# Kernel optimization log

Measured on AMD Instinct MI355X. Metric: run time of the kernel, lower is better.

Reference implementation:

```python
import jax, jax.numpy as jnp
import numpy as np
from jax import lax

PAD_IDX = 0
SOS_IDX = 1


def gru_cell(x, h, w_ih, w_hh, b_ih, b_hh):
    # PyTorch GRU cell: gates ordered [r, z, n]
    gi = x @ w_ih.T + b_ih            # [B, 3H]
    gh = h @ w_hh.T + b_hh            # [B, 3H]
    i_r, i_z, i_n = jnp.split(gi, 3, axis=-1)
    h_r, h_z, h_n = jnp.split(gh, 3, axis=-1)
    r = jax.nn.sigmoid(i_r + h_r)
    z = jax.nn.sigmoid(i_z + h_z)
    n = jnp.tanh(i_n + r * h_n)
    return (1.0 - z) * n + z * h


def setup_inputs() -> dict:
    key = jax.random.key(0)
    ks = jax.random.split(key, 24)
    B, S, T = 32, 64, 48
    Vs, Vt, E, H = 32000, 32000, 512, 1024
    sH = 1.0 / np.sqrt(H)
    sE = 1.0 / np.sqrt(E)

    def p(k, shape, scale):
        return jax.random.normal(k, shape, jnp.float32) * scale

    inp = {
        'source_ids': jax.random.randint(ks[0], (B, S), 0, Vs),
        'target_ids': jax.random.randint(ks[1], (B, T), 0, Vt),
        'enc_embed': p(ks[2], (Vs, E), 0.02).at[PAD_IDX].set(0.0),
        'enc_w_ih': p(ks[3], (3 * H, E), sE),
        'enc_w_hh': p(ks[4], (3 * H, H), sH),
        'enc_b_ih': p(ks[5], (3 * H,), sH),
        'enc_b_hh': p(ks[6], (3 * H,), sH),
        'wq': p(ks[7], (H, H), sH),
        'bq': p(ks[8], (H,), sH),
        'wk': p(ks[9], (H, H), sH),
        'bk': p(ks[10], (H,), sH),
        'ws': p(ks[11], (H,), sH),
        'bs': p(ks[12], (), sH),
        'dec_embed': p(ks[13], (Vt, E), 0.02).at[PAD_IDX].set(0.0),
        'dec_w_ih': p(ks[14], (3 * H, E + H), sH),
        'dec_w_hh': p(ks[15], (3 * H, H), sH),
        'dec_b_ih': p(ks[16], (3 * H,), sH),
        'dec_b_hh': p(ks[17], (3 * H,), sH),
        'wo': p(ks[18], (Vt, H), sH),
        'bo': p(ks[19], (Vt,), sH),
    }
    return inp


def reference(source_ids, target_ids, enc_embed, enc_w_ih, enc_w_hh, enc_b_ih,
              enc_b_hh, wq, bq, wk, bk, ws, bs, dec_embed, dec_w_ih, dec_w_hh,
              dec_b_ih, dec_b_hh, wo, bo):
    B, S = source_ids.shape
    T = target_ids.shape[1]
    H = wq.shape[0]

    # ----- encoder GRU -----
    enc_emb = enc_embed[source_ids]                  # [B,S,E] (dropout = identity, eval)
    h0 = jnp.zeros((B, H), enc_emb.dtype)

    def enc_step(h, x):
        h = gru_cell(x, h, enc_w_ih, enc_w_hh, enc_b_ih, enc_b_hh)
        return h, h

    h_final, enc_out = lax.scan(enc_step, h0, enc_emb.transpose(1, 0, 2))
    enc_out = enc_out.transpose(1, 0, 2)             # [B,S,H]

    mask = source_ids != PAD_IDX                     # [B,S]
    keys_proj = enc_out @ wk.T + bk                  # [B,S,H] (hoisted; linear, step-invariant)

    # ----- decoder with teacher forcing (ratio=1.0 => always teacher) -----
    dec_in = jnp.concatenate(
        [jnp.full((B, 1), SOS_IDX, dtype=target_ids.dtype), target_ids[:, 1:T - 1]],
        axis=1)                                      # [B,T-1]
    dec_emb = dec_embed[dec_in].transpose(1, 0, 2)   # [T-1,B,E]

    def dec_step(h, emb):
        q = h @ wq.T + bq                            # [B,H]
        scores = jnp.tanh(q[:, None, :] + keys_proj) @ ws + bs   # [B,S]
        scores = jnp.where(mask, scores, -jnp.inf)
        w = jax.nn.softmax(scores, axis=-1)          # [B,S]
        ctx = jnp.einsum('bs,bsh->bh', w, enc_out)   # [B,H]
        x = jnp.concatenate([emb, ctx], axis=-1)     # [B,E+H]
        h2 = gru_cell(x, h, dec_w_ih, dec_w_hh, dec_b_ih, dec_b_hh)
        logits = h2 @ wo.T + bo                      # [B,V]
        return h2, (logits, w)

    _, (logits, attn) = lax.scan(dec_step, h_final, dec_emb)
    logits = logits.transpose(1, 0, 2)               # [B,T-1,V]
    attn = attn.transpose(1, 0, 2)                   # [B,T-1,S]
    return logits, attn
```

## Files before the change

kernel.cpp:

```cpp
#include <hip/hip_runtime.h>


#define BB 32
#define SS 64
#define TT 48
#define TD 47
#define EE 512
#define HH 1024
#define GG 3072
#define VV 32000
#define SOS_IDX 1
#define MPAD 1536

typedef float f32x4 __attribute__((ext_vector_type(4)));
typedef short bf16x8 __attribute__((ext_vector_type(8)));

static __device__ __forceinline__ float sigmoid_f(float x) {
    return 1.0f / (1.0f + __expf(-x));
}
static __device__ __forceinline__ float tanh_f(float x) {
    return 1.0f - 2.0f / (__expf(2.0f * x) + 1.0f);
}
static __device__ __forceinline__ unsigned short f2bf(float f) {
    unsigned u = __float_as_uint(f);
    u = u + 0x7fffu + ((u >> 16) & 1u);
    return (unsigned short)(u >> 16);
}
static __device__ __forceinline__ void cst4(float* p, f32x4 v) {
    asm volatile("global_store_dwordx4 %0, %1, off sc0 sc1" :: "v"(p), "v"(v) : "memory");
}
static __device__ __forceinline__ void cst1(float* p, float v) {
    asm volatile("global_store_dword %0, %1, off sc0 sc1" :: "v"(p), "v"(v) : "memory");
}

static __device__ __forceinline__ void gbar(int* bar, int leafsz, int& bstep) {
    asm volatile("s_waitcnt vmcnt(0) lgkmcnt(0)" ::: "memory");
    __syncthreads();
    bstep += 1;
    if (threadIdx.x == 0) {
        int* leaf = bar + (blockIdx.x & 7) * 32;
        int* root = bar + 512;
        int lv = __hip_atomic_fetch_add(leaf, 1, __ATOMIC_RELAXED, __HIP_MEMORY_SCOPE_AGENT) + 1;
        if (lv == bstep * leafsz) {
            __hip_atomic_fetch_add(root, 1, __ATOMIC_RELAXED, __HIP_MEMORY_SCOPE_AGENT);
        }
        while (__hip_atomic_load(root, __ATOMIC_RELAXED, __HIP_MEMORY_SCOPE_AGENT) < bstep * 8) {
            __builtin_amdgcn_s_sleep(1);
        }
    }
    __syncthreads();
    asm volatile("" ::: "memory");
}

__global__ void k_dec_idx(const int* __restrict__ tgt, int* __restrict__ idx) {
    int m = blockIdx.x * 256 + threadIdx.x;
    if (m < TD * BB) {
        int t = m >> 5, b = m & 31;
        idx[m] = (t == 0) ? SOS_IDX : tgt[b * TT + t];
    }
}

__global__ __launch_bounds__(256) void k_gemm128(
    const float* __restrict__ A, const float* __restrict__ Wt,
    const float* __restrict__ bias, float* __restrict__ C,
    const int* __restrict__ rowidx,
    int M, int N, int K, int lda, int ldw, int ldc)
{
    __shared__ __align__(16) float As[16][128];
    __shared__ __align__(16) float Bs[16][128];
    const int tid = threadIdx.x;
    const int tm = tid >> 4, tn = tid & 15;
    const int row0 = blockIdx.y * 128;
    const int col0 = blockIdx.x * 128;
    const int lr = tid >> 1;
    const int lq = tid & 1;

    long arow_off = -1;
    {
        int arow = row0 + lr;
        if (arow < M) {
            int r = rowidx ? rowidx[arow] : arow;
            arow_off = (long)r * lda;
        }
    }
    const long wrow_off = (long)(col0 + lr) * ldw;

    float acc[8][8];
#pragma unroll
    for (int i = 0; i < 8; ++i)
#pragma unroll
        for (int j = 0; j < 8; ++j) acc[i][j] = 0.f;

    for (int k0 = 0; k0 < K; k0 += 16) {
        f32x4 av0 = {0.f,0.f,0.f,0.f}, av1 = {0.f,0.f,0.f,0.f};
        if (arow_off >= 0) {
            av0 = *(const f32x4*)(A + arow_off + k0 + lq * 8);
            av1 = *(const f32x4*)(A + arow_off + k0 + lq * 8 + 4);
        }
        f32x4 wv0 = *(const f32x4*)(Wt + wrow_off + k0 + lq * 8);
        f32x4 wv1 = *(const f32x4*)(Wt + wrow_off + k0 + lq * 8 + 4);
        __syncthreads();
#pragma unroll
        for (int i = 0; i < 4; ++i) {
            As[lq * 8 + i][lr] = av0[i];
            As[lq * 8 + 4 + i][lr] = av1[i];
            Bs[lq * 8 + i][lr] = wv0[i];
            Bs[lq * 8 + 4 + i][lr] = wv1[i];
        }
        __syncthreads();
#pragma unroll
        for (int kk = 0; kk < 16; ++kk) {
            f32x4 a0 = *(const f32x4*)&As[kk][tm * 4];
            f32x4 a1 = *(const f32x4*)&As[kk][64 + tm * 4];
            f32x4 b0 = *(const f32x4*)&Bs[kk][tn * 4];
            f32x4 b1 = *(const f32x4*)&Bs[kk][64 + tn * 4];
            float a[8], b[8];
#pragma unroll
            for (int i = 0; i < 4; ++i) {
                a[i] = a0[i]; a[4 + i] = a1[i];
                b[i] = b0[i]; b[4 + i] = b1[i];
            }
#pragma unroll
            for (int i = 0; i < 8; ++i)
#pragma unroll
                for (int j = 0; j < 8; ++j) acc[i][j] += a[i] * b[j];
        }
    }

    f32x4 bv0 = {0.f,0.f,0.f,0.f}, bv1 = {0.f,0.f,0.f,0.f};
    if (bias) {
        bv0 = *(const f32x4*)(bias + col0 + tn * 4);
        bv1 = *(const f32x4*)(bias + col0 + 64 + tn * 4);
    }
#pragma unroll
    for (int i = 0; i < 8; ++i) {
        int m = row0 + ((i < 4) ? (tm * 4 + i) : (64 + tm * 4 + i - 4));
        if (m >= M) continue;
        f32x4 v0, v1;
#pragma unroll
        for (int j = 0; j < 4; ++j) {
            v0[j] = acc[i][j] + bv0[j];
            v1[j] = acc[i][4 + j] + bv1[j];
        }
        *(f32x4*)(C + (long)m * ldc + col0 + tn * 4) = v0;
        *(f32x4*)(C + (long)m * ldc + col0 + 64 + tn * 4) = v1;
    }
}

__global__ __launch_bounds__(256) void k_cvtA(
    const float* __restrict__ A, unsigned short* __restrict__ Ah,
    unsigned short* __restrict__ Al)
{
    size_t i4 = ((size_t)blockIdx.x * 256 + threadIdx.x) * 4;
    int row = (int)(i4 >> 10);
    f32x4 v = {0.f, 0.f, 0.f, 0.f};
    if (row < TD * BB) v = *(const f32x4*)(A + i4);
    ushort4 h, l;
    float hf;
    h.x = f2bf(v.x); hf = __uint_as_float((unsigned)h.x << 16); l.x = f2bf(v.x - hf);
    h.y = f2bf(v.y); hf = __uint_as_float((unsigned)h.y << 16); l.y = f2bf(v.y - hf);
    h.z = f2bf(v.z); hf = __uint_as_float((unsigned)h.z << 16); l.z = f2bf(v.z - hf);
    h.w = f2bf(v.w); hf = __uint_as_float((unsigned)h.w << 16); l.w = f2bf(v.w - hf);
    *(ushort4*)(Ah + i4) = h;
    *(ushort4*)(Al + i4) = l;
}

__global__ __launch_bounds__(256) void k_cvtB(
    const float* __restrict__ Bsrc, unsigned short* __restrict__ Bh)
{
    size_t i4 = ((size_t)blockIdx.x * 256 + threadIdx.x) * 4;
    f32x4 v = *(const f32x4*)(Bsrc + i4);
    ushort4 h;
    h.x = f2bf(v.x); h.y = f2bf(v.y); h.z = f2bf(v.z); h.w = f2bf(v.w);
    *(ushort4*)(Bh + i4) = h;
}

__global__ __launch_bounds__(256) void k_mfma_logits(
    const unsigned short* __restrict__ Ah,
    const unsigned short* __restrict__ Bh,
    const float* __restrict__ bo, float* __restrict__ C)
{
    __shared__ __align__(16) unsigned short As[128 * 64];
    __shared__ __align__(16) unsigned short Bs[128 * 64];
    const int tid = threadIdx.x;
    const int m0 = blockIdx.y * 128;
    const int n0 = blockIdx.x * 128;
    const int r = tid >> 1, half = tid & 1;
    const int lane = tid & 63, wid = tid >> 6;
    const int wm = wid >> 1, wn = wid & 1;

    f32x4 acc[4][4];
#pragma unroll
    for (int i = 0; i < 4; ++i)
#pragma unroll
        for (int j = 0; j < 4; ++j) acc[i][j] = (f32x4){0.f, 0.f, 0.f, 0.f};

    char* AsB = (char*)As;
    char* BsB = (char*)Bs;
    const int lwb = r * 128 + half * 64;
    const int swz = (r & 7) << 4;

    for (int kt = 0; kt < 32; ++kt) {
        const int kb = (kt & 15) * 64;
        const unsigned short* Ap = Ah + ((kt >> 4) ? (size_t)MPAD * 1024 : 0)
                                 + (size_t)(m0 + r) * 1024 + kb + half * 32;
        const unsigned short* Bp = Bh + (size_t)(n0 + r) * 1024 + kb + half * 32;
        f32x4 a0 = *(const f32x4*)(Ap + 0);
        f32x4 a1 = *(const f32x4*)(Ap + 8);
        f32x4 a2 = *(const f32x4*)(Ap + 16);
        f32x4 a3 = *(const f32x4*)(Ap + 24);
        f32x4 b0 = *(const f32x4*)(Bp + 0);
        f32x4 b1 = *(const f32x4*)(Bp + 8);
        f32x4 b2 = *(const f32x4*)(Bp + 16);
        f32x4 b3 = *(const f32x4*)(Bp + 24);
        __syncthreads();
        *(f32x4*)(AsB + ((lwb + 0)  ^ swz)) = a0;
        *(f32x4*)(AsB + ((lwb + 16) ^ swz)) = a1;
        *(f32x4*)(AsB + ((lwb + 32) ^ swz)) = a2;
        *(f32x4*)(AsB + ((lwb + 48) ^ swz)) = a3;
        *(f32x4*)(BsB + ((lwb + 0)  ^ swz)) = b0;
        *(f32x4*)(BsB + ((lwb + 16) ^ swz)) = b1;
        *(f32x4*)(BsB + ((lwb + 32) ^ swz)) = b2;
        *(f32x4*)(BsB + ((lwb + 48) ^ swz)) = b3;
        __syncthreads();
#pragma unroll
        for (int ks = 0; ks < 2; ++ks) {
            bf16x8 af[4], bf[4];
#pragma unroll
            for (int u = 0; u < 4; ++u) {
                int ml = wm * 64 + u * 16 + (lane & 15);
                int byteA = ml * 128 + ks * 64 + ((lane >> 4) << 4);
                af[u] = *(const bf16x8*)(AsB + (byteA ^ ((ml & 7) << 4)));
                int nl = wn * 64 + u * 16 + (lane & 15);
                int byteB = nl * 128 + ks * 64 + ((lane >> 4) << 4);
                bf[u] = *(const bf16x8*)(BsB + (byteB ^ ((nl & 7) << 4)));
            }
#pragma unroll
            for (int mi = 0; mi < 4; ++mi)
#pragma unroll
                for (int ni = 0; ni < 4; ++ni)
                    acc[mi][ni] = __builtin_amdgcn_mfma_f32_16x16x32_bf16(
                        af[mi], bf[ni], acc[mi][ni], 0, 0, 0);
        }
    }

    const int cl = lane & 15, rq = lane >> 4;
#pragma unroll
    for (int ni = 0; ni < 4; ++ni) {
        int col = n0 + wn * 64 + ni * 16 + cl;
        float bias = bo[col];
#pragma unroll
        for (int mi = 0; mi < 4; ++mi) {
#pragma unroll
            for (int j = 0; j < 4; ++j) {
                int m = m0 + wm * 64 + mi * 16 + rq * 4 + j;
                if (m < TD * BB) {
                    int orow = (m & 31) * TD + (m >> 5);
                    C[(size_t)orow * VV + col] = acc[mi][ni][j] + bias;
                }
            }
        }
    }
}

__global__ __launch_bounds__(512, 2) void k_enc_steps(
    const float* __restrict__ gi, const float* __restrict__ Whh,
    const float* __restrict__ bhh, float* __restrict__ enc_out,
    int s0, int ns, int* bar)
{
    __shared__ float red[12][16][32];
    __shared__ float sums[12][32];
    const int tid = threadIdx.x, bid = blockIdx.x;
    const int b = tid & 31, ks = tid >> 5;
    const int j0 = bid * 4;
    const int kc = ks * 64;
    int bstep = 0;

    for (int ss = 0; ss < ns; ++ss) {
        const int s = s0 + ss;
        float acc[12];
#pragma unroll
        for (int u = 0; u < 12; ++u) acc[u] = 0.f;
        if (s > 0) {
            f32x4 hreg[16];
            const float* hb = enc_out + ((size_t)b * SS + (s - 1)) * HH + kc;
#pragma unroll
            for (int i = 0; i < 16; ++i) hreg[i] = *(const f32x4*)(hb + (i << 2));
#pragma unroll
            for (int jj = 0; jj < 4; ++jj) {
                const float* pr = Whh + ((size_t)(j0 + jj) << 10) + kc;
                const float* pz = Whh + ((size_t)(HH + j0 + jj) << 10) + kc;
                const float* pn = Whh + ((size_t)(2 * HH + j0 + jj) << 10) + kc;
                float ar = 0.f, az = 0.f, an = 0.f;
#pragma unroll
                for (int i = 0; i < 16; ++i) {
                    f32x4 h4 = hreg[i];
                    f32x4 w;
                    w = *(const f32x4*)(pr + (i << 2));
                    ar += h4.x * w.x + h4.y * w.y + h4.z * w.z + h4.w * w.w;
                    w = *(const f32x4*)(pz + (i << 2));
                    az += h4.x * w.x + h4.y * w.y + h4.z * w.z + h4.w * w.w;
                    w = *(const f32x4*)(pn + (i << 2));
                    an += h4.x * w.x + h4.y * w.y + h4.z * w.z + h4.w * w.w;
                }
                acc[jj] = ar; acc[4 + jj] = az; acc[8 + jj] = an;
            }
        }
#pragma unroll
        for (int u = 0; u < 12; ++u) red[u][ks][b] = acc[u];
        __syncthreads();
        if (tid < 384) {
            int u = tid >> 5, fb = tid & 31;
            float x = 0.f;
#pragma unroll
            for (int q = 0; q < 16; ++q) x += red[u][q][fb];
            sums[u][fb] = x;
        }
        __syncthreads();
        if (tid < 32) {
            const f32x4 bh0 = *(const f32x4*)(bhh + j0);
            const f32x4 bh1 = *(const f32x4*)(bhh + HH + j0);
            const f32x4 bh2 = *(const f32x4*)(bhh + 2 * HH + j0);
            const float* gr = gi + (size_t)(tid * SS + s) * GG;
            f32x4 g0 = *(const f32x4*)(gr + j0);
            f32x4 g1 = *(const f32x4*)(gr + HH + j0);
            f32x4 g2 = *(const f32x4*)(gr + 2 * HH + j0);
            f32x4 hold = {0.f, 0.f, 0.f, 0.f};
            if (s > 0) hold = *(const f32x4*)(enc_out + ((size_t)tid * SS + (s - 1)) * HH + j0);
            f32x4 hn;
#pragma unroll
            for (int e = 0; e < 4; ++e) {
                float r = sigmoid_f(g0[e] + sums[e][tid] + bh0[e]);
                float z = sigmoid_f(g1[e] + sums[4 + e][tid] + bh1[e]);
                float n = tanh_f(g2[e] + r * (sums[8 + e][tid] + bh2[e]));
                hn[e] = (1.f - z) * n + z * hold[e];
            }
            cst4(enc_out + ((size_t)tid * SS + s) * HH + j0, hn);
        }
        if (ss != ns - 1) gbar(bar, 256 / 8, bstep);
    }
}

__global__ __launch_bounds__(512, 2) void k_dec_step(
    const float* __restrict__ hbase, long hstride,
    const float* __restrict__ Whh, const float* __restrict__ wq,
    const float* __restrict__ bq, const float* __restrict__ keys,
    const float* __restrict__ wsv, const float* __restrict__ bsv,
    const int* __restrict__ src, const float* __restrict__ encproj,
    const float* __restrict__ gi, const float* __restrict__ bhh,
    float* __restrict__ q2, float* __restrict__ hsums2,
    float* __restrict__ h2all, float* __restrict__ attn_out,
    int t, int* bar)
{
    __shared__ float red[16][16][32];
    __shared__ float qsum[4][32];
    const int tid = threadIdx.x, bid = blockIdx.x;
    const int b = tid & 31, ks = tid >> 5;
    const int j0 = bid * 4;
    const int kc = ks * 64;
    int bstep = 0;

    {
        f32x4 hreg[16];
        const float* hb = hbase + (size_t)b * hstride + kc;
#pragma unroll
        for (int i = 0; i < 16; ++i) hreg[i] = *(const f32x4*)(hb + (i << 2));
        float acc[16];
#pragma unroll
        for (int jj = 0; jj < 4; ++jj) {
            const float* pr = Whh + ((size_t)(j0 + jj) << 10) + kc;
            const float* pz = Whh + ((size_t)(HH + j0 + jj) << 10) + kc;
            const float* pn = Whh + ((size_t)(2 * HH + j0 + jj) << 10) + kc;
            const float* pq = wq + ((size_t)(j0 + jj) << 10) + kc;
            float ar = 0.f, az = 0.f, an = 0.f, aq = 0.f;
#pragma unroll
            for (int i = 0; i < 16; ++i) {
                f32x4 h4 = hreg[i];
                f32x4 w;
                w = *(const f32x4*)(pr + (i << 2));
                ar += h4.x * w.x + h4.y * w.y + h4.z * w.z + h4.w * w.w;
                w = *(const f32x4*)(pz + (i << 2));
                az += h4.x * w.x + h4.y * w.y + h4.z * w.z + h4.w * w.w;
                w = *(const f32x4*)(pn + (i << 2));
                an += h4.x * w.x + h4.y * w.y + h4.z * w.z + h4.w * w.w;
                w = *(const f32x4*)(pq + (i << 2));
                aq += h4.x * w.x + h4.y * w.y + h4.z * w.z + h4.w * w.w;
            }
            acc[jj] = ar; acc[4 + jj] = az; acc[8 + jj] = an; acc[12 + jj] = aq;
        }
#pragma unroll
        for (int u = 0; u < 16; ++u) red[u][ks][b] = acc[u];
        __syncthreads();
        {
            int u = tid >> 5, fb = tid & 31;
            float x = 0.f;
#pragma unroll
            for (int q = 0; q < 16; ++q) x += red[u][q][fb];
            if (u < 12) cst1(hsums2 + (size_t)bid * 384 + u * 32 + fb, x);
            else qsum[u - 12][fb] = x;
        }
        __syncthreads();
        if (tid < 32) {
            const f32x4 bq4 = *(const f32x4*)(bq + j0);
            f32x4 qv;
            qv.x = qsum[0][tid] + bq4.x;
            qv.y = qsum[1][tid] + bq4.y;
            qv.z = qsum[2][tid] + bq4.z;
            qv.w = qsum[3][tid] + bq4.w;
            cst4(q2 + (size_t)bid * 128 + tid * 4, qv);
        }
    }
    gbar(bar, 256 / 8, bstep);

    const int ab = bid & 31, part = bid >> 5;
    float* qs  = &red[0][0][0];
    float* wss = qs + 1024;
    float* scs = wss + 1024;
    float* wl  = scs + 512;
    float* xls = wl + 64;
    if (tid < 256) {
        f32x4 qv = *(const f32x4*)(q2 + (size_t)tid * 128 + ab * 4);
        f32x4 wv = *(const f32x4*)(wsv + tid * 4);
        *(f32x4*)&qs[tid * 4] = qv;
        *(f32x4*)&wss[tid * 4] = wv;
    }
    __syncthreads();
    {
        const int s4 = tid >> 3, kq = tid & 7;
        const float* kr = keys + (size_t)(ab * SS + s4) * HH + kq * 128;
        float a = 0.f;
        for (int i = 0; i < 32; ++i) {
            f32x4 kv = *(const f32x4*)(kr + (i << 2));
            int k = kq * 128 + (i << 2);
            a += tanh_f(qs[k] + kv.x) * wss[k]
               + tanh_f(qs[k + 1] + kv.y) * wss[k + 1]
               + tanh_f(qs[k + 2] + kv.z) * wss[k + 2]
               + tanh_f(qs[k + 3] + kv.w) * wss[k + 3];
        }
        scs[kq * 64 + s4] = a;
    }
    __syncthreads();
    if (tid < 64) {
        float v = bsv[0];
#pragma unroll
        for (int q = 0; q < 8; ++q) v += scs[q * 64 + tid];
        bool valid = src[ab * SS + tid] != 0;
        float m = valid ? v : -3.0e38f;
        for (int off = 32; off; off >>= 1) m = fmaxf(m, __shfl_xor(m, off));
        float e = valid ? __expf(v - m) : 0.f;
        float ssum = e;
        for (int off = 32; off; off >>= 1) ssum += __shfl_xor(ssum, off);
        float wgt = e / ssum;
        wl[tid] = wgt;
        if (part == 0)
            attn_out[((size_t)ab * TD + t) * SS + tid] = wgt;
    }
    __syncthreads();
    if (tid < 384) {
        int gate = tid >> 7, jj = tid & 127;
        int col = (gate << 10) + (part << 7) + jj;
        float xa = 0.f;
        const float* ep = encproj + (size_t)ab * SS * GG + col;
        for (int s2 = 0; s2 < 64; ++s2)
            xa += wl[s2] * ep[(size_t)s2 * GG];
        xls[tid] = xa;
    }
    __syncthreads();
    if (tid < 128) {
        const int j = (part << 7) + tid;
        const int wbid = (part << 5) + (tid >> 2);
        const int jj = tid & 3;
        const float* hs = hsums2 + (size_t)wbid * 384;
        float sh0 = hs[(0 * 4 + jj) * 32 + ab];
        float sh1 = hs[(1 * 4 + jj) * 32 + ab];
        float sh2 = hs[(2 * 4 + jj) * 32 + ab];
        const float* gr = gi + (size_t)(t * BB + ab) * GG;
        float r = sigmoid_f(gr[j] + xls[tid] + sh0 + bhh[j]);
        float z = sigmoid_f(gr[HH + j] + xls[128 + tid] + sh1 + bhh[HH + j]);
        float n = tanh_f(gr[2 * HH + j] + xls[256 + tid] + r * (sh2 + bhh[2 * HH + j]));
        float hold = hbase[(size_t)ab * hstride + j];
        h2all[((size_t)t * BB + ab) * HH + j] = (1.f - z) * n + z * hold;
    }
}

extern "C" void kernel_launch(void* const* d_in, const int* in_sizes, int n_in,
                              void* d_out, int out_size, void* d_ws, size_t ws_size,
                              hipStream_t stream)
{
    const int*   src  = (const int*)d_in[0];
    const int*   tgt  = (const int*)d_in[1];
    const float* eemb = (const float*)d_in[2];
    const float* ewih = (const float*)d_in[3];
    const float* ewhh = (const float*)d_in[4];
    const float* ebih = (const float*)d_in[5];
    const float* ebhh = (const float*)d_in[6];
    const float* wq   = (const float*)d_in[7];
    const float* bq   = (const float*)d_in[8];
    const float* wk   = (const float*)d_in[9];
    const float* bk   = (const float*)d_in[10];
    const float* wsv  = (const float*)d_in[11];
    const float* bsv  = (const float*)d_in[12];
    const float* demb = (const float*)d_in[13];
    const float* dwih = (const float*)d_in[14];
    const float* dwhh = (const float*)d_in[15];
    const float* dbih = (const float*)d_in[16];
    const float* dbhh = (const float*)d_in[17];
    const float* wo   = (const float*)d_in[18];
    const float* bo   = (const float*)d_in[19];
    float* out = (float*)d_out;

    float* w = (float*)d_ws;
    float* enc_gi  = w;
    float* dec_gi  = enc_gi  + (size_t)BB * SS * GG;
    float* enc_out = dec_gi  + (size_t)TD * BB * GG;
    float* keys    = enc_out + (size_t)BB * SS * HH;
    float* h2all   = keys    + (size_t)BB * SS * HH;
    float* q2      = h2all   + (size_t)TD * BB * HH;
    float* hsums2  = q2      + (size_t)256 * 128;
    int*   didx    = (int*)(hsums2 + (size_t)256 * 384);
    int*   barAll  = didx + TD * BB + 32;
    unsigned short* Ah = (unsigned short*)(barAll + 63 * 576 + 32);
    unsigned short* Al = Ah + (size_t)MPAD * 1024;
    unsigned short* Bh = (unsigned short*)w;

    float* encproj = enc_gi;
    float* attn_out = out + (size_t)BB * TD * VV;

    hipMemsetAsync(barAll, 0, 63 * 576 * sizeof(int), stream);
    k_dec_idx<<<dim3((TD * BB + 255) / 256), 256, 0, stream>>>(tgt, didx);

    k_gemm128<<<dim3(GG / 128, (BB * SS) / 128), 256, 0, stream>>>(
        eemb, ewih, ebih, enc_gi, src, BB * SS, GG, EE, EE, EE, GG);
    k_gemm128<<<dim3(GG / 128, (TD * BB + 127) / 128), 256, 0, stream>>>(
        demb, dwih, dbih, dec_gi, didx, TD * BB, GG, EE, EE, EE + HH, GG);

    for (int i = 0; i < 16; ++i)
        k_enc_steps<<<dim3(256), dim3(512), 0, stream>>>(
            enc_gi, ewhh, ebhh, enc_out, i * 4, 4, barAll + i * 576);

    k_gemm128<<<dim3(HH / 128, (BB * SS) / 128), 256, 0, stream>>>(
        enc_out, wk, bk, keys, nullptr, BB * SS, HH, HH, HH, HH, HH);
    k_gemm128<<<dim3(GG / 128, (BB * SS) / 128), 256, 0, stream>>>(
        enc_out, dwih + EE, nullptr, encproj, nullptr,
        BB * SS, GG, HH, HH, EE + HH, GG);

    for (int t = 0; t < TD; ++t) {
        const float* hbase = (t == 0) ? enc_out + (size_t)(SS - 1) * HH
                                      : h2all + (size_t)(t - 1) * BB * HH;
        long hstride = (t == 0) ? (long)SS * HH : (long)HH;
        k_dec_step<<<dim3(256), dim3(512), 0, stream>>>(
            hbase, hstride, dwhh, wq, bq, keys, wsv, bsv, src, encproj,
            dec_gi, dbhh, q2, hsums2, h2all, attn_out, t, barAll + (16 + t) * 576);
    }

    k_cvtA<<<dim3(MPAD * 1024 / 1024), 256, 0, stream>>>(h2all, Ah, Al);
    k_cvtB<<<dim3(VV * 1024 / 1024), 256, 0, stream>>>(wo, Bh);
    k_mfma_logits<<<dim3(VV / 128, MPAD / 128), 256, 0, stream>>>(
        Ah, Bh, bo, out);
}
```

Before: 4.588 ms.

## Make encoder and decoder recurrences persistent kernels with grid barriers

Replaces the 16 encoder launches and 47 per-step decoder launches with one persistent kernel each, which loops over all timesteps and synchronises through the existing atomic grid barrier. Cross-block values (q2, hsums2, h2all) are now read and written with cache-bypassing loads and stores so they stay visible between steps without a kernel boundary. The ws vector is loaded into shared memory once per kernel rather than once per step. This removes per-launch overhead and the launch gaps between steps, but it depends on all 256 blocks being resident at once and adds one extra barrier per decoder step.

```diff
diff --git a/kernel.cpp b/kernel.cpp
--- a/kernel.cpp
+++ b/kernel.cpp
@@ -31,6 +31,20 @@
 }
 static __device__ __forceinline__ void cst1(float* p, float v) {
     asm volatile("global_store_dword %0, %1, off sc0 sc1" :: "v"(p), "v"(v) : "memory");
+}
+static __device__ __forceinline__ f32x4 cld4(const float* p) {
+    f32x4 v;
+    asm volatile("global_load_dwordx4 %0, %1, off sc0 sc1" : "=v"(v) : "v"(p) : "memory");
+    return v;
+}
+static __device__ __forceinline__ float cld1f(const float* p) {
+    float v;
+    asm volatile("global_load_dword %0, %1, off sc0 sc1" : "=v"(v) : "v"(p) : "memory");
+    return v;
+}
+static __device__ __forceinline__ void cwait() {
+    asm volatile("s_waitcnt vmcnt(0)" ::: "memory");
+    __builtin_amdgcn_sched_barrier(0);
 }
 
 static __device__ __forceinline__ void gbar(int* bar, int leafsz, int& bstep) {
@@ -263,10 +277,9 @@
     }
 }
 
-__global__ __launch_bounds__(512, 2) void k_enc_steps(
+__global__ __launch_bounds__(512, 2) void k_enc_all(
     const float* __restrict__ gi, const float* __restrict__ Whh,
-    const float* __restrict__ bhh, float* __restrict__ enc_out,
-    int s0, int ns, int* bar)
+    const float* __restrict__ bhh, float* __restrict__ enc_out, int* bar)
 {
     __shared__ float red[12][16][32];
     __shared__ float sums[12][32];
@@ -276,8 +289,7 @@
     const int kc = ks * 64;
     int bstep = 0;
 
-    for (int ss = 0; ss < ns; ++ss) {
-        const int s = s0 + ss;
+    for (int s = 0; s < SS; ++s) {
         float acc[12];
 #pragma unroll
         for (int u = 0; u < 12; ++u) acc[u] = 0.f;
@@ -337,149 +349,160 @@
             }
             cst4(enc_out + ((size_t)tid * SS + s) * HH + j0, hn);
         }
-        if (ss != ns - 1) gbar(bar, 256 / 8, bstep);
-    }
-}
-
-__global__ __launch_bounds__(512, 2) void k_dec_step(
-    const float* __restrict__ hbase, long hstride,
-    const float* __restrict__ Whh, const float* __restrict__ wq,
-    const float* __restrict__ bq, const float* __restrict__ keys,
-    const float* __restrict__ wsv, const float* __restrict__ bsv,
-    const int* __restrict__ src, const float* __restrict__ encproj,
-    const float* __restrict__ gi, const float* __restrict__ bhh,
-    float* __restrict__ q2, float* __restrict__ hsums2,
-    float* __restrict__ h2all, float* __restrict__ attn_out,
-    int t, int* bar)
+        if (s != SS - 1) gbar(bar, 256 / 8, bstep);
+    }
+}
+
+__global__ __launch_bounds__(512, 2) void k_dec_all(
+    const float* __restrict__ enc_out, const float* __restrict__ Whh,
+    const float* __restrict__ wq, const float* __restrict__ bq,
+    const float* __restrict__ keys, const float* __restrict__ wsv,
+    const float* __restrict__ bsv, const int* __restrict__ src,
+    const float* __restrict__ encproj, const float* __restrict__ gi,
+    const float* __restrict__ bhh, float* __restrict__ q2,
+    float* __restrict__ hsums2, float* __restrict__ h2all,
+    float* __restrict__ attn_out, int* bar)
 {
     __shared__ float red[16][16][32];
     __shared__ float qsum[4][32];
+    __shared__ float wss[HH];
     const int tid = threadIdx.x, bid = blockIdx.x;
     const int b = tid & 31, ks = tid >> 5;
     const int j0 = bid * 4;
     const int kc = ks * 64;
+    const int ab = bid & 31, part = bid >> 5;
     int bstep = 0;
 
-    {
-        f32x4 hreg[16];
-        const float* hb = hbase + (size_t)b * hstride + kc;
-#pragma unroll
-        for (int i = 0; i < 16; ++i) hreg[i] = *(const f32x4*)(hb + (i << 2));
-        float acc[16];
-#pragma unroll
-        for (int jj = 0; jj < 4; ++jj) {
-            const float* pr = Whh + ((size_t)(j0 + jj) << 10) + kc;
-            const float* pz = Whh + ((size_t)(HH + j0 + jj) << 10) + kc;
-            const float* pn = Whh + ((size_t)(2 * HH + j0 + jj) << 10) + kc;
-            const float* pq = wq + ((size_t)(j0 + jj) << 10) + kc;
-            float ar = 0.f, az = 0.f, an = 0.f, aq = 0.f;
-#pragma unroll
-            for (int i = 0; i < 16; ++i) {
-                f32x4 h4 = hreg[i];
-                f32x4 w;
-                w = *(const f32x4*)(pr + (i << 2));
-                ar += h4.x * w.x + h4.y * w.y + h4.z * w.z + h4.w * w.w;
-                w = *(const f32x4*)(pz + (i << 2));
-                az += h4.x * w.x + h4.y * w.y + h4.z * w.z + h4.w * w.w;
-                w = *(const f32x4*)(pn + (i << 2));
-                an += h4.x * w.x + h4.y * w.y + h4.z * w.z + h4.w * w.w;
-                w = *(const f32x4*)(pq + (i << 2));
-                aq += h4.x * w.x + h4.y * w.y + h4.z * w.z + h4.w * w.w;
-            }
-            acc[jj] = ar; acc[4 + jj] = az; acc[8 + jj] = an; acc[12 + jj] = aq;
-        }
-#pragma unroll
-        for (int u = 0; u < 16; ++u) red[u][ks][b] = acc[u];
-        __syncthreads();
+    if (tid < 256)
+        *(f32x4*)&wss[tid * 4] = *(const f32x4*)(wsv + tid * 4);
+    const f32x4 bq4 = *(const f32x4*)(bq + j0);
+
+    for (int t = 0; t < TD; ++t) {
+        const float* hbase = (t == 0) ? enc_out + (size_t)(SS - 1) * HH
+                                      : h2all + (size_t)(t - 1) * BB * HH;
+        const long hstride = (t == 0) ? (long)SS * HH : (long)HH;
+
         {
-            int u = tid >> 5, fb = tid & 31;
-            float x = 0.f;
-#pragma unroll
-            for (int q = 0; q < 16; ++q) x += red[u][q][fb];
-            if (u < 12) cst1(hsums2 + (size_t)bid * 384 + u * 32 + fb, x);
-            else qsum[u - 12][fb] = x;
-        }
-        __syncthreads();
-        if (tid < 32) {
-            const f32x4 bq4 = *(const f32x4*)(bq + j0);
-            f32x4 qv;
-            qv.x = qsum[0][tid] + bq4.x;
-            qv.y = qsum[1][tid] + bq4.y;
-            qv.z = qsum[2][tid] + bq4.z;
-            qv.w = qsum[3][tid] + bq4.w;
-            cst4(q2 + (size_t)bid * 128 + tid * 4, qv);
-        }
-    }
-    gbar(bar, 256 / 8, bstep);
-
-    const int ab = bid & 31, part = bid >> 5;
-    float* qs  = &red[0][0][0];
-    float* wss = qs + 1024;
-    float* scs = wss + 1024;
-    float* wl  = scs + 512;
-    float* xls = wl + 64;
-    if (tid < 256) {
-        f32x4 qv = *(const f32x4*)(q2 + (size_t)tid * 128 + ab * 4);
-        f32x4 wv = *(const f32x4*)(wsv + tid * 4);
-        *(f32x4*)&qs[tid * 4] = qv;
-        *(f32x4*)&wss[tid * 4] = wv;
-    }
-    __syncthreads();
-    {
-        const int s4 = tid >> 3, kq = tid & 7;
-        const float* kr = keys + (size_t)(ab * SS + s4) * HH + kq * 128;
-        float a = 0.f;
-        for (int i = 0; i < 32; ++i) {
-            f32x4 kv = *(const f32x4*)(kr + (i << 2));
-            int k = kq * 128 + (i << 2);
-            a += tanh_f(qs[k] + kv.x) * wss[k]
-               + tanh_f(qs[k + 1] + kv.y) * wss[k + 1]
-               + tanh_f(qs[k + 2] + kv.z) * wss[k + 2]
-               + tanh_f(qs[k + 3] + kv.w) * wss[k + 3];
-        }
-        scs[kq * 64 + s4] = a;
-    }
-    __syncthreads();
-    if (tid < 64) {
-        float v = bsv[0];
-#pragma unroll
-        for (int q = 0; q < 8; ++q) v += scs[q * 64 + tid];
-        bool valid = src[ab * SS + tid] != 0;
-        float m = valid ? v : -3.0e38f;
-        for (int off = 32; off; off >>= 1) m = fmaxf(m, __shfl_xor(m, off));
-        float e = valid ? __expf(v - m) : 0.f;
-        float ssum = e;
-        for (int off = 32; off; off >>= 1) ssum += __shfl_xor(ssum, off);
-        float wgt = e / ssum;
-        wl[tid] = wgt;
-        if (part == 0)
-            attn_out[((size_t)ab * TD + t) * SS + tid] = wgt;
-    }
-    __syncthreads();
-    if (tid < 384) {
-        int gate = tid >> 7, jj = tid & 127;
-        int col = (gate << 10) + (part << 7) + jj;
-        float xa = 0.f;
-        const float* ep = encproj + (size_t)ab * SS * GG + col;
-        for (int s2 = 0; s2 < 64; ++s2)
-            xa += wl[s2] * ep[(size_t)s2 * GG];
-        xls[tid] = xa;
-    }
-    __syncthreads();
-    if (tid < 128) {
-        const int j = (part << 7) + tid;
-        const int wbid = (part << 5) + (tid >> 2);
-        const int jj = tid & 3;
-        const float* hs = hsums2 + (size_t)wbid * 384;
-        float sh0 = hs[(0 * 4 + jj) * 32 + ab];
-        float sh1 = hs[(1 * 4 + jj) * 32 + ab];
-        float sh2 = hs[(2 * 4 + jj) * 32 + ab];
-        const float* gr = gi + (size_t)(t * BB + ab) * GG;
-        float r = sigmoid_f(gr[j] + xls[tid] + sh0 + bhh[j]);
-        float z = sigmoid_f(gr[HH + j] + xls[128 + tid] + sh1 + bhh[HH + j]);
-        float n = tanh_f(gr[2 * HH + j] + xls[256 + tid] + r * (sh2 + bhh[2 * HH + j]));
-        float hold = hbase[(size_t)ab * hstride + j];
-        h2all[((size_t)t * BB + ab) * HH + j] = (1.f - z) * n + z * hold;
+            f32x4 hreg[16];
+            const float* hb = hbase + (size_t)b * hstride + kc;
+#pragma unroll
+            for (int i = 0; i < 16; ++i) hreg[i] = *(const f32x4*)(hb + (i << 2));
+            float acc[16];
+#pragma unroll
+            for (int jj = 0; jj < 4; ++jj) {
+                const float* pr = Whh + ((size_t)(j0 + jj) << 10) + kc;
+                const float* pz = Whh + ((size_t)(HH + j0 + jj) << 10) + kc;
+                const float* pn = Whh + ((size_t)(2 * HH + j0 + jj) << 10) + kc;
+                const float* pq = wq + ((size_t)(j0 + jj) << 10) + kc;
+                float ar = 0.f, az = 0.f, an = 0.f, aq = 0.f;
+#pragma unroll
+                for (int i = 0; i < 16; ++i) {
+                    f32x4 h4 = hreg[i];
+                    f32x4 w;
+                    w = *(const f32x4*)(pr + (i << 2));
+                    ar += h4.x * w.x + h4.y * w.y + h4.z * w.z + h4.w * w.w;
+                    w = *(const f32x4*)(pz + (i << 2));
+                    az += h4.x * w.x + h4.y * w.y + h4.z * w.z + h4.w * w.w;
+                    w = *(const f32x4*)(pn + (i << 2));
+                    an += h4.x * w.x + h4.y * w.y + h4.z * w.z + h4.w * w.w;
+                    w = *(const f32x4*)(pq + (i << 2));
+                    aq += h4.x * w.x + h4.y * w.y + h4.z * w.z + h4.w * w.w;
+                }
+                acc[jj] = ar; acc[4 + jj] = az; acc[8 + jj] = an; acc[12 + jj] = aq;
+            }
+#pragma unroll
+            for (int u = 0; u < 16; ++u) red[u][ks][b] = acc[u];
+            __syncthreads();
+            {
+                int u = tid >> 5, fb = tid & 31;
+                float x = 0.f;
+#pragma unroll
+                for (int q = 0; q < 16; ++q) x += red[u][q][fb];
+                if (u < 12) cst1(hsums2 + (size_t)bid * 384 + u * 32 + fb, x);
+                else qsum[u - 12][fb] = x;
+            }
+            __syncthreads();
+            if (tid < 32) {
+                f32x4 qv;
+                qv.x = qsum[0][tid] + bq4.x;
+                qv.y = qsum[1][tid] + bq4.y;
+                qv.z = qsum[2][tid] + bq4.z;
+                qv.w = qsum[3][tid] + bq4.w;
+                cst4(q2 + (size_t)bid * 128 + tid * 4, qv);
+            }
+        }
+        gbar(bar, 256 / 8, bstep);
+
+        {
+            float* qs  = &red[0][0][0];
+            float* scs = qs + 1024;
+            float* wl  = scs + 512;
+            float* xls = wl + 64;
+            if (tid < 256) {
+                f32x4 qv = cld4(q2 + (size_t)tid * 128 + ab * 4);
+                cwait();
+                *(f32x4*)&qs[tid * 4] = qv;
+            }
+            __syncthreads();
+            {
+                const int s4 = tid >> 3, kq = tid & 7;
+                const float* kr = keys + (size_t)(ab * SS + s4) * HH + kq * 128;
+                float a = 0.f;
+                for (int i = 0; i < 32; ++i) {
+                    f32x4 kv = *(const f32x4*)(kr + (i << 2));
+                    int k = kq * 128 + (i << 2);
+                    a += tanh_f(qs[k] + kv.x) * wss[k]
+                       + tanh_f(qs[k + 1] + kv.y) * wss[k + 1]
+                       + tanh_f(qs[k + 2] + kv.z) * wss[k + 2]
+                       + tanh_f(qs[k + 3] + kv.w) * wss[k + 3];
+                }
+                scs[kq * 64 + s4] = a;
+            }
+            __syncthreads();
+            if (tid < 64) {
+                float v = bsv[0];
+#pragma unroll
+                for (int q = 0; q < 8; ++q) v += scs[q * 64 + tid];
+                bool valid = src[ab * SS + tid] != 0;
+                float m = valid ? v : -3.0e38f;
+                for (int off = 32; off; off >>= 1) m = fmaxf(m, __shfl_xor(m, off));
+                float e = valid ? __expf(v - m) : 0.f;
+                float ssum = e;
+                for (int off = 32; off; off >>= 1) ssum += __shfl_xor(ssum, off);
+                float wgt = e / ssum;
+                wl[tid] = wgt;
+                if (part == 0)
+                    attn_out[((size_t)ab * TD + t) * SS + tid] = wgt;
+            }
+            __syncthreads();
+            if (tid < 384) {
+                int gate = tid >> 7, jj = tid & 127;
+                int col = (gate << 10) + (part << 7) + jj;
+                float xa = 0.f;
+                const float* ep = encproj + (size_t)ab * SS * GG + col;
+                for (int s2 = 0; s2 < 64; ++s2)
+                    xa += wl[s2] * ep[(size_t)s2 * GG];
+                xls[tid] = xa;
+            }
+            __syncthreads();
+            if (tid < 128) {
+                const int j = (part << 7) + tid;
+                const int wbid = (part << 5) + (tid >> 2);
+                const int jj = tid & 3;
+                const float* hs = hsums2 + (size_t)wbid * 384;
+                float sh0 = cld1f(hs + (0 * 4 + jj) * 32 + ab);
+                float sh1 = cld1f(hs + (1 * 4 + jj) * 32 + ab);
+                float sh2 = cld1f(hs + (2 * 4 + jj) * 32 + ab);
+                cwait();
+                const float* gr = gi + (size_t)(t * BB + ab) * GG;
+                float r = sigmoid_f(gr[j] + xls[tid] + sh0 + bhh[j]);
+                float z = sigmoid_f(gr[HH + j] + xls[128 + tid] + sh1 + bhh[HH + j]);
+                float n = tanh_f(gr[2 * HH + j] + xls[256 + tid] + r * (sh2 + bhh[2 * HH + j]));
+                float hold = hbase[(size_t)ab * hstride + j];
+                cst1(h2all + ((size_t)t * BB + ab) * HH + j, (1.f - z) * n + z * hold);
+            }
+        }
+        if (t != TD - 1) gbar(bar, 256 / 8, bstep);
     }
 }
 
@@ -519,14 +542,14 @@
     float* hsums2  = q2      + (size_t)256 * 128;
     int*   didx    = (int*)(hsums2 + (size_t)256 * 384);
     int*   barAll  = didx + TD * BB + 32;
-    unsigned short* Ah = (unsigned short*)(barAll + 63 * 576 + 32);
+    unsigned short* Ah = (unsigned short*)(barAll + 2 * 576 + 32);
     unsigned short* Al = Ah + (size_t)MPAD * 1024;
     unsigned short* Bh = (unsigned short*)w;
 
     float* encproj = enc_gi;
     float* attn_out = out + (size_t)BB * TD * VV;
 
-    hipMemsetAsync(barAll, 0, 63 * 576 * sizeof(int), stream);
+    hipMemsetAsync(barAll, 0, 2 * 576 * sizeof(int), stream);
     k_dec_idx<<<dim3((TD * BB + 255) / 256), 256, 0, stream>>>(tgt, didx);
 
     k_gemm128<<<dim3(GG / 128, (BB * SS) / 128), 256, 0, stream>>>(
@@ -534,9 +557,8 @@
     k_gemm128<<<dim3(GG / 128, (TD * BB + 127) / 128), 256, 0, stream>>>(
         demb, dwih, dbih, dec_gi, didx, TD * BB, GG, EE, EE, EE + HH, GG);
 
-    for (int i = 0; i < 16; ++i)
-        k_enc_steps<<<dim3(256), dim3(512), 0, stream>>>(
-            enc_gi, ewhh, ebhh, enc_out, i * 4, 4, barAll + i * 576);
+    k_enc_all<<<dim3(256), dim3(512), 0, stream>>>(
+        enc_gi, ewhh, ebhh, enc_out, barAll);
 
     k_gemm128<<<dim3(HH / 128, (BB * SS) / 128), 256, 0, stream>>>(
         enc_out, wk, bk, keys, nullptr, BB * SS, HH, HH, HH, HH, HH);
@@ -544,14 +566,9 @@
         enc_out, dwih + EE, nullptr, encproj, nullptr,
         BB * SS, GG, HH, HH, EE + HH, GG);
 
-    for (int t = 0; t < TD; ++t) {
-        const float* hbase = (t == 0) ? enc_out + (size_t)(SS - 1) * HH
-                                      : h2all + (size_t)(t - 1) * BB * HH;
-        long hstride = (t == 0) ? (long)SS * HH : (long)HH;
-        k_dec_step<<<dim3(256), dim3(512), 0, stream>>>(
-            hbase, hstride, dwhh, wq, bq, keys, wsv, bsv, src, encproj,
-            dec_gi, dbhh, q2, hsums2, h2all, attn_out, t, barAll + (16 + t) * 576);
-    }
+    k_dec_all<<<dim3(256), dim3(512), 0, stream>>>(
+        enc_out, dwhh, wq, bq, keys, wsv, bsv, src, encproj,
+        dec_gi, dbhh, q2, hsums2, h2all, attn_out, barAll + 576);
 
     k_cvtA<<<dim3(MPAD * 1024 / 1024), 256, 0, stream>>>(h2all, Ah, Al);
     k_cvtB<<<dim3(VV * 1024 / 1024), 256, 0, stream>>>(wo, Bh);
```

New measurement: 12.08 ms. +163.3%, slower.
